# Kernel tuning notes

Hardware: AMD Instinct MI355X
Metric: run time of the kernel (lower is better)

Reference implementation:

```python
import jax, jax.numpy as jnp
import numpy as np

EMBED_DIM = 768
NUM_HEADS = 12
HEAD_DIM = EMBED_DIM // NUM_HEADS


def setup_inputs() -> dict:
    key = jax.random.key(0)
    k_x, k_qkv_w, k_qkv_b, k_pw, k_pb = jax.random.split(key, 5)
    B, S = 16, 1024
    scale = 1.0 / np.sqrt(EMBED_DIM)
    return {
        "x": jax.random.normal(k_x, (B, S, EMBED_DIM), dtype=jnp.float32),
        "qkv_w": jax.random.normal(k_qkv_w, (EMBED_DIM, 3 * EMBED_DIM), dtype=jnp.float32) * scale,
        "qkv_b": jax.random.normal(k_qkv_b, (3 * EMBED_DIM,), dtype=jnp.float32) * 0.02,
        "proj_w": jax.random.normal(k_pw, (EMBED_DIM, EMBED_DIM), dtype=jnp.float32) * scale,
        "proj_b": jax.random.normal(k_pb, (EMBED_DIM,), dtype=jnp.float32) * 0.02,
    }


def reference(x, qkv_w, qkv_b, proj_w, proj_b):
    B, S, E = x.shape
    H, D = NUM_HEADS, HEAD_DIM
    qkv = x @ qkv_w + qkv_b                      # [B, S, 3E]
    qkv = qkv.reshape(B, S, 3, H, D)
    qkv = jnp.transpose(qkv, (2, 0, 3, 1, 4))    # [3, B, H, S, D]
    q, k, v = qkv[0], qkv[1], qkv[2]
    scores = jnp.einsum("bhqd,bhkd->bhqk", q, k) / jnp.sqrt(jnp.float32(D))
    probs = jax.nn.softmax(scores, axis=-1)      # dropout is identity in eval
    attn = jnp.einsum("bhqk,bhkd->bhqd", probs, v)
    attn = jnp.transpose(attn, (0, 2, 1, 3)).reshape(B, S, E)
    return attn @ proj_w + proj_b
```

## Files before the change

kernel.cpp:

```cpp
#include <hip/hip_runtime.h>
#include <hip/hip_bf16.h>

typedef unsigned short u16;
typedef short s16x8 __attribute__((ext_vector_type(8)));
typedef float f32x4 __attribute__((ext_vector_type(4)));

#define EMB 768
#define NH 12
#define HD 64
#define BB 16
#define SS 1024
#define MTOK (BB*SS)
#define NQKV (3*EMB)
#define QSZ ((size_t)BB*NH*SS*HD)

#define GLOBAL_AS const __attribute__((address_space(1))) void*
#define LDS_AS __attribute__((address_space(3))) void*

#if __has_builtin(__builtin_amdgcn_exp2f)
#define EXP2(x) __builtin_amdgcn_exp2f(x)
#else
#define EXP2(x) exp2f(x)
#endif

__device__ __forceinline__ u16 f2bf(float f){
  unsigned u = __float_as_uint(f);
  u += 0x7FFFu + ((u >> 16) & 1u);
  return (u16)(u >> 16);
}
__device__ __forceinline__ u16 f2bf_trunc(float f){
  return (u16)(__float_as_uint(f) >> 16);
}
__device__ __forceinline__ f32x4 mfma16(s16x8 a, s16x8 b, f32x4 c){
  return __builtin_amdgcn_mfma_f32_16x16x32_bf16(a, b, c, 0, 0, 0);
}

#define NBA 12288
#define NBB 1728
#define NBC 576

__device__ __forceinline__ void transpose_body(
    u16 (*tile)[33], const float* __restrict__ in, u16* __restrict__ out,
    int R, int C, int bxi, int byi){
  int bx = bxi * 32, by = byi * 32;
  int tx = threadIdx.x & 31, ty = threadIdx.x >> 5;
  #pragma unroll
  for(int i = 0; i < 32; i += 8)
    tile[ty + i][tx] = f2bf(in[(size_t)(by + ty + i) * C + bx + tx]);
  __syncthreads();
  #pragma unroll
  for(int i = 0; i < 32; i += 8)
    out[(size_t)(bx + ty + i) * R + by + tx] = tile[tx][ty + i];
}

__global__ __launch_bounds__(256) void prep_kernel(
    const float4* __restrict__ x4, ushort4* __restrict__ xb4,
    const float* __restrict__ qkv_w, u16* __restrict__ qkv_wT,
    const float* __restrict__ proj_w, u16* __restrict__ proj_wT){
  __shared__ u16 tile[32][33];
  int bid = blockIdx.x;
  if(bid < NBA){
    int i = bid * 256 + threadIdx.x;
    float4 f = x4[i];
    ushort4 o;
    o.x = f2bf(f.x); o.y = f2bf(f.y); o.z = f2bf(f.z); o.w = f2bf(f.w);
    xb4[i] = o;
  } else if(bid < NBA + NBB){
    int bi = bid - NBA;
    transpose_body(tile, qkv_w, qkv_wT, EMB, NQKV, bi % (NQKV/32), bi / (NQKV/32));
  } else {
    int bi = bid - NBA - NBB;
    transpose_body(tile, proj_w, proj_wT, EMB, EMB, bi % (EMB/32), bi / (EMB/32));
  }
}

template<int MODE>
__device__ __forceinline__ void gemm_body(
    const u16* __restrict__ A, const u16* __restrict__ Bt,
    const float* __restrict__ bias,
    void* __restrict__ out0, u16* __restrict__ out1, u16* __restrict__ out2){
  const int K = 768, NT = 12;
  __shared__ u16 As[2][256*64];
  __shared__ u16 Bs[2][256*64];
  int tid = threadIdx.x;

  int gx = gridDim.x;
  int nwg = gx * gridDim.y;
  int L = blockIdx.y * gx + blockIdx.x;
  int nl = (L & 7) * (nwg >> 3) + (L >> 3);
  int m0 = (nl / gx) * 256, n0 = (nl % gx) * 256;

  int w = tid >> 6, lane = tid & 63, quad = lane >> 4, l15 = lane & 15;
  int wm = (w >> 2) * 128, wn = (w & 3) * 64;
  int rr = lane >> 3;
  int cp = lane & 7;
  f32x4 acc[8][4] = {};

  auto stage = [&](int t){
    int d = t & 1, k0 = t * 64;
    #pragma unroll
    for(int it = 0; it < 4; ++it){
      int ci = it * 8 + w;
      int r  = ci * 8 + rr;
      int gc = (cp ^ (r & 7)) * 8;
      __builtin_amdgcn_global_load_lds(
          (GLOBAL_AS)(A + (size_t)(m0 + r) * K + k0 + gc),
          (LDS_AS)(As[d] + ci * 512 + lane * 8), 16, 0, 0);
      __builtin_amdgcn_global_load_lds(
          (GLOBAL_AS)(Bt + (size_t)(n0 + r) * K + k0 + gc),
          (LDS_AS)(Bs[d] + ci * 512 + lane * 8), 16, 0, 0);
    }
  };

  stage(0); stage(1);
  asm volatile("s_waitcnt vmcnt(8)" ::: "memory");
  __builtin_amdgcn_s_barrier();

  s16x8 a[4], b[4];
  #pragma unroll
  for(int t = 0; t < NT; ++t){
    int d = t & 1;
    #pragma unroll
    for(int ph = 0; ph < 4; ++ph){
      int kk = ph >> 1, mh = ph & 1;
      int ch = ((kk * 4 + quad) ^ (l15 & 7)) * 8;
      if(mh == 0){
        #pragma unroll
        for(int nt = 0; nt < 4; ++nt)
          b[nt] = *(const s16x8*)&Bs[d][(wn + nt*16 + l15) * 64 + ch];
      }
      #pragma unroll
      for(int i = 0; i < 4; ++i)
        a[i] = *(const s16x8*)&As[d][(wm + (mh*4 + i)*16 + l15) * 64 + ch];
      __builtin_amdgcn_s_setprio(1);
      #pragma unroll
      for(int i = 0; i < 4; ++i)
        #pragma unroll
        for(int nt = 0; nt < 4; ++nt)
          acc[mh*4 + i][nt] = mfma16(a[i], b[nt], acc[mh*4 + i][nt]);
      __builtin_amdgcn_s_setprio(0);
    }
    if(t < NT - 1){
      __builtin_amdgcn_s_barrier();
      if(t + 2 < NT){
        stage(t + 2);
        asm volatile("s_waitcnt vmcnt(8)" ::: "memory");
      } else {
        asm volatile("s_waitcnt vmcnt(0)" ::: "memory");
      }
      __builtin_amdgcn_s_barrier();
    }
  }

  #pragma unroll
  for(int mt = 0; mt < 8; ++mt){
    #pragma unroll
    for(int nt = 0; nt < 4; ++nt){
      int n = n0 + wn + nt*16 + l15;
      float bv = bias[n];
      #pragma unroll
      for(int r = 0; r < 4; ++r){
        int m = m0 + wm + mt*16 + quad*4 + r;
        float v = acc[mt][nt][r] + bv;
        if(MODE == 1){
          ((float*)out0)[(size_t)m * EMB + n] = v;
        } else {
          u16 hv = f2bf(v);
          int which = n / EMB, rem = n - which * EMB;
          int h = rem >> 6, d = rem & 63;
          int bb = m >> 10, ss = m & 1023;
          size_t bh = (size_t)(bb * NH + h);
          if(which == 0)      ((u16*)out0)[(bh * SS + ss) * HD + d] = hv;
          else if(which == 1) out1[(bh * SS + ss) * HD + d] = hv;
          else                out2[(bh * HD + d) * SS + ss] = hv;
        }
      }
    }
  }
}

__global__ __launch_bounds__(512, 2) void qkv_gemm_kernel(
    const u16* __restrict__ A, const u16* __restrict__ Bt,
    const float* __restrict__ bias,
    u16* __restrict__ Qo, u16* __restrict__ Ko, u16* __restrict__ Vo){
  gemm_body<0>(A, Bt, bias, Qo, Ko, Vo);
}
__global__ __launch_bounds__(512, 2) void proj_gemm_kernel(
    const u16* __restrict__ A, const u16* __restrict__ Bt,
    const float* __restrict__ bias, float* __restrict__ out){
  gemm_body<1>(A, Bt, bias, out, nullptr, nullptr);
}

__global__ __launch_bounds__(256) void attn_kernel(
    const u16* __restrict__ Qws, const u16* __restrict__ Kws,
    const u16* __restrict__ Vtws, u16* __restrict__ attn){
  __shared__ u16 Ks[2][64*64];
  __shared__ u16 Vs[2][64*64];
  __shared__ __align__(16) u16 Ps[4][2][16][76];
  int tid = threadIdx.x;
  int w = tid >> 6, lane = tid & 63, quad = lane >> 4, l15 = lane & 15;
  int bh = blockIdx.x;
  int b = bh / NH, h = bh - b * NH;
  int q0 = blockIdx.y * 128 + w * 32;
  const u16* Qbase = Qws  + (size_t)bh * SS * HD;
  const u16* Kbase = Kws  + (size_t)bh * SS * HD;
  const u16* Vbase = Vtws + (size_t)bh * HD * SS;

  s16x8 aq[2][2];
  #pragma unroll
  for(int m = 0; m < 2; m++){
    int qrow = q0 + m*16 + l15;
    #pragma unroll
    for(int kk = 0; kk < 2; kk++)
      aq[m][kk] = *(const s16x8*)(Qbase + (size_t)qrow * HD + kk*32 + quad*8);
  }

  f32x4 o[2][4] = {};
  float psum[2][4] = {};
  const float C1 = 0.125f * 1.44269504f;
  const float C0 = -30.0f * 1.44269504f;

  int krr = lane >> 3, kcp = lane & 7;

  auto stageKV = [&](int p, int kt){
    #pragma unroll
    for(int it = 0; it < 2; ++it){
      int ins = it * 4 + w;
      int r   = ins * 8 + krr;
      int gck = (kcp ^ (r & 7)) * 8;
      __builtin_amdgcn_global_load_lds(
          (GLOBAL_AS)(Kbase + (size_t)(kt*64 + r) * HD + gck),
          (LDS_AS)(Ks[p] + ins * 512 + lane * 8), 16, 0, 0);
      __builtin_amdgcn_global_load_lds(
          (GLOBAL_AS)(Vbase + (size_t)r * SS + kt*64 + gck),
          (LDS_AS)(Vs[p] + ins * 512 + lane * 8), 16, 0, 0);
    }
  };

  stageKV(0, 0);
  int p = 0;
  for(int kt = 0; kt < 16; ++kt){
    __syncthreads();
    if(kt < 15) stageKV(p ^ 1, kt + 1);

    #pragma unroll
    for(int nt = 0; nt < 4; ++nt){
      s16x8 bk[2];
      #pragma unroll
      for(int kk = 0; kk < 2; kk++){
        int ch = ((kk*4 + quad) ^ (l15 & 7)) * 8;
        bk[kk] = *(const s16x8*)&Ks[p][(nt*16 + l15) * 64 + ch];
      }
      #pragma unroll
      for(int m = 0; m < 2; m++){
        f32x4 z = {};
        z = mfma16(aq[m][0], bk[0], z);
        z = mfma16(aq[m][1], bk[1], z);
        #pragma unroll
        for(int r = 0; r < 4; r++){
          float pv = EXP2(z[r] * C1 + C0);
          psum[m][r] += pv;
          Ps[w][m][quad*4 + r][nt*16 + l15] = f2bf_trunc(pv);
        }
      }
    }
    #pragma unroll
    for(int k4 = 0; k4 < 2; k4++){
      s16x8 pa[2];
      #pragma unroll
      for(int m = 0; m < 2; m++)
        pa[m] = *(const s16x8*)&Ps[w][m][l15][k4*32 + quad*8];
      #pragma unroll
      for(int nt = 0; nt < 4; nt++){
        int ch = ((k4*4 + quad) ^ (l15 & 7)) * 8;
        s16x8 vb = *(const s16x8*)&Vs[p][(nt*16 + l15) * 64 + ch];
        #pragma unroll
        for(int m = 0; m < 2; m++)
          o[m][nt] = mfma16(pa[m], vb, o[m][nt]);
      }
    }
    p ^= 1;
  }

  #pragma unroll
  for(int m = 0; m < 2; m++){
    #pragma unroll
    for(int r = 0; r < 4; r++){
      float s = psum[m][r];
      s += __shfl_xor(s, 1, 64);
      s += __shfl_xor(s, 2, 64);
      s += __shfl_xor(s, 4, 64);
      s += __shfl_xor(s, 8, 64);
      float inv = 1.0f / s;
      int srow = q0 + m*16 + quad*4 + r;
      size_t base = ((size_t)(b * SS + srow)) * EMB + h * HD;
      #pragma unroll
      for(int nt = 0; nt < 4; nt++)
        attn[base + nt*16 + l15] = f2bf(o[m][nt][r] * inv);
    }
  }
}

extern "C" void kernel_launch(void* const* d_in, const int* in_sizes, int n_in,
                              void* d_out, int out_size, void* d_ws, size_t ws_size,
                              hipStream_t stream){
  const float* x      = (const float*)d_in[0];
  const float* qkv_w  = (const float*)d_in[1];
  const float* qkv_b  = (const float*)d_in[2];
  const float* proj_w = (const float*)d_in[3];
  const float* proj_b = (const float*)d_in[4];

  char* ws = (char*)d_ws;
  u16* qkv_wT  = (u16*)ws; ws += (size_t)NQKV * EMB * 2;
  u16* proj_wT = (u16*)ws; ws += (size_t)EMB * EMB * 2;
  u16* x_bf = (u16*)ws; ws += QSZ * 2;
  u16* Qws  = (u16*)ws; ws += QSZ * 2;
  u16* Kws  = (u16*)ws; ws += QSZ * 2;
  u16* Vtws = (u16*)ws; ws += QSZ * 2;
  u16* attn = x_bf;

  prep_kernel<<<NBA + NBB + NBC, 256, 0, stream>>>(
      (const float4*)x, (ushort4*)x_bf, qkv_w, qkv_wT, proj_w, proj_wT);
  qkv_gemm_kernel<<<dim3(NQKV/256, MTOK/256), 512, 0, stream>>>(
      x_bf, qkv_wT, qkv_b, Qws, Kws, Vtws);
  attn_kernel<<<dim3(BB*NH, SS/128), 256, 0, stream>>>(Qws, Kws, Vtws, attn);
  proj_gemm_kernel<<<dim3(EMB/256, MTOK/256), 512, 0, stream>>>(
      attn, proj_wT, proj_b, (float*)d_out);
}
```

Baseline: 314.9 us.

## Restructure GEMM main loop into 8-phase quadrant schedule with interleaved staging

Rewrites the GEMM K-loop so each 64-wide K tile is split into four quadrant phases (mh, nh), each with its own LDS reads, barrier-fenced MFMA block, and a quarter-slice of the next tile's global-to-LDS loads. Global loads are issued as finer chunks spread across phases rather than in one burst per tile. The goal is to overlap memory traffic with MFMA work and keep matrix units busy, in the style of ping-pong schedules. In exchange it adds many more barriers per tile and sched_barrier fences, which could serialize waves and hurt overlap if the phases are unbalanced.

```diff
diff --git a/kernel.cpp b/kernel.cpp
--- a/kernel.cpp
+++ b/kernel.cpp
@@ -96,61 +96,100 @@
   int cp = lane & 7;
   f32x4 acc[8][4] = {};
 
-  auto stage = [&](int t){
+  auto stageQ = [&](int t, int q){
     int d = t & 1, k0 = t * 64;
-    #pragma unroll
-    for(int it = 0; it < 4; ++it){
-      int ci = it * 8 + w;
+    const u16* src = (q < 2) ? A : Bt;
+    int base = (q < 2) ? m0 : n0;
+    u16* dst = (q < 2) ? As[d] : Bs[d];
+    int h = q & 1;
+    #pragma unroll
+    for(int it = 0; it < 2; ++it){
+      int ci = h*16 + it*8 + w;
       int r  = ci * 8 + rr;
       int gc = (cp ^ (r & 7)) * 8;
       __builtin_amdgcn_global_load_lds(
-          (GLOBAL_AS)(A + (size_t)(m0 + r) * K + k0 + gc),
-          (LDS_AS)(As[d] + ci * 512 + lane * 8), 16, 0, 0);
-      __builtin_amdgcn_global_load_lds(
-          (GLOBAL_AS)(Bt + (size_t)(n0 + r) * K + k0 + gc),
-          (LDS_AS)(Bs[d] + ci * 512 + lane * 8), 16, 0, 0);
-    }
-  };
-
-  stage(0); stage(1);
-  asm volatile("s_waitcnt vmcnt(8)" ::: "memory");
-  __builtin_amdgcn_s_barrier();
-
-  s16x8 a[4], b[4];
-  #pragma unroll
-  for(int t = 0; t < NT; ++t){
-    int d = t & 1;
-    #pragma unroll
-    for(int ph = 0; ph < 4; ++ph){
-      int kk = ph >> 1, mh = ph & 1;
-      int ch = ((kk * 4 + quad) ^ (l15 & 7)) * 8;
-      if(mh == 0){
-        #pragma unroll
-        for(int nt = 0; nt < 4; ++nt)
-          b[nt] = *(const s16x8*)&Bs[d][(wn + nt*16 + l15) * 64 + ch];
-      }
+          (GLOBAL_AS)(src + (size_t)(base + r) * K + k0 + gc),
+          (LDS_AS)(dst + ci * 512 + lane * 8), 16, 0, 0);
+    }
+  };
+
+  s16x8 a[8], b0[4], b1[4];
+  auto dsA = [&](int d, int mh){
+    #pragma unroll
+    for(int kk = 0; kk < 2; ++kk){
+      int ch = ((kk*4 + quad) ^ (l15 & 7)) * 8;
       #pragma unroll
       for(int i = 0; i < 4; ++i)
-        a[i] = *(const s16x8*)&As[d][(wm + (mh*4 + i)*16 + l15) * 64 + ch];
-      __builtin_amdgcn_s_setprio(1);
+        a[kk*4+i] = *(const s16x8*)&As[d][(wm + (mh*4+i)*16 + l15) * 64 + ch];
+    }
+  };
+  auto dsB = [&](int d, int nh, s16x8* bb){
+    #pragma unroll
+    for(int kk = 0; kk < 2; ++kk){
+      int ch = ((kk*4 + quad) ^ (l15 & 7)) * 8;
+      #pragma unroll
+      for(int j = 0; j < 2; ++j)
+        bb[kk*2+j] = *(const s16x8*)&Bs[d][(wn + (nh*2+j)*16 + l15) * 64 + ch];
+    }
+  };
+  auto mfmaQ = [&](int mh, int nh, const s16x8* bb){
+    __builtin_amdgcn_s_setprio(1);
+    #pragma unroll
+    for(int kk = 0; kk < 2; ++kk)
       #pragma unroll
       for(int i = 0; i < 4; ++i)
         #pragma unroll
-        for(int nt = 0; nt < 4; ++nt)
-          acc[mh*4 + i][nt] = mfma16(a[i], b[nt], acc[mh*4 + i][nt]);
-      __builtin_amdgcn_s_setprio(0);
-    }
-    if(t < NT - 1){
-      __builtin_amdgcn_s_barrier();
-      if(t + 2 < NT){
-        stage(t + 2);
-        asm volatile("s_waitcnt vmcnt(8)" ::: "memory");
-      } else {
-        asm volatile("s_waitcnt vmcnt(0)" ::: "memory");
-      }
-      __builtin_amdgcn_s_barrier();
-    }
-  }
+        for(int j = 0; j < 2; ++j)
+          acc[mh*4+i][nh*2+j] = mfma16(a[kk*4+i], bb[kk*2+j], acc[mh*4+i][nh*2+j]);
+    __builtin_amdgcn_s_setprio(0);
+  };
+
+#define PHASE_SYNC() do{ \
+    __builtin_amdgcn_s_barrier(); \
+    asm volatile("s_waitcnt lgkmcnt(0)" ::: "memory"); \
+    __builtin_amdgcn_sched_barrier(0); \
+  }while(0)
+#define PHASE_END() do{ \
+    __builtin_amdgcn_s_barrier(); \
+    __builtin_amdgcn_sched_barrier(0); \
+  }while(0)
+
+  stageQ(0,0); stageQ(0,1); stageQ(0,2); stageQ(0,3);
+  stageQ(1,0);
+  asm volatile("s_waitcnt vmcnt(2)" ::: "memory");
+  __builtin_amdgcn_s_barrier();
+  __builtin_amdgcn_sched_barrier(0);
+
+  #pragma unroll
+  for(int j = 0; j < NT/2; ++j){
+    int t = 2*j;
+    stageQ(t+1, 1);
+    dsA(0, 0); dsB(0, 0, b0);
+    PHASE_SYNC(); mfmaQ(0, 0, b0); PHASE_END();
+    stageQ(t+1, 2);
+    dsB(0, 1, b1);
+    PHASE_SYNC(); mfmaQ(0, 1, b1); PHASE_END();
+    stageQ(t+1, 3);
+    dsA(0, 1);
+    PHASE_SYNC(); mfmaQ(1, 0, b0); PHASE_END();
+    if(t+2 < NT){ stageQ(t+2, 0); asm volatile("s_waitcnt vmcnt(2)" ::: "memory"); }
+    else        { asm volatile("s_waitcnt vmcnt(0)" ::: "memory"); }
+    PHASE_SYNC(); mfmaQ(1, 1, b1); PHASE_END();
+    if(t+2 < NT) stageQ(t+2, 1);
+    dsA(1, 0); dsB(1, 0, b0);
+    PHASE_SYNC(); mfmaQ(0, 0, b0); PHASE_END();
+    if(t+2 < NT) stageQ(t+2, 2);
+    dsB(1, 1, b1);
+    PHASE_SYNC(); mfmaQ(0, 1, b1); PHASE_END();
+    if(t+2 < NT) stageQ(t+2, 3);
+    dsA(1, 1);
+    PHASE_SYNC(); mfmaQ(1, 0, b0); PHASE_END();
+    if(t+3 < NT){ stageQ(t+3, 0); asm volatile("s_waitcnt vmcnt(2)" ::: "memory"); }
+    else if(t+2 < NT){ asm volatile("s_waitcnt vmcnt(0)" ::: "memory"); }
+    PHASE_SYNC(); mfmaQ(1, 1, b1); PHASE_END();
+  }
+#undef PHASE_SYNC
+#undef PHASE_END
 
   #pragma unroll
   for(int mt = 0; mt < 8; ++mt){
```

Measured after the change: 316.3 us. No clear change (+0.4%).
